# Performance work log

Hardware: AMD Instinct MI355X
Metric: run time of the kernel (lower is better)

The kernel has to match this reference:

```python
import jax, jax.numpy as jnp
import numpy as np

IN_CH = (512, 1024, 512, 256, 256, 256)
CORR = 9          # patch_size of spatial_correlation_sample
UP = 1            # upsample_param
BASE = 96         # level-0 spatial size
B = 2
NEG_SLOPE = 0.01  # nn.LeakyReLU default


def _upsample_nearest(x, s):
    # nearest upsample by integer factor s (matches nn.Upsample(mode='nearest'))
    if s == 1:
        return x
    return jnp.repeat(jnp.repeat(x, s, axis=2), s, axis=3)


def _downsample_nearest(x, s):
    # nearest 'upsample' with scale 1/s: out[d] = in[d*s]
    if s == 1:
        return x
    return x[:, :, ::s, ::s]


def _spatial_correlation(f1, f2, patch):
    # kernel_size=1, stride=1, padding=0, dilation_patch=1, zero pad for
    # out-of-bounds displacements. Returns [b, patch*patch, h, w]
    r = patch // 2
    b, c, h, w = f1.shape
    f2p = jnp.pad(f2, ((0, 0), (0, 0), (r, r), (r, r)))
    vols = [jnp.einsum('bchw,bchw->bhw', f1, f2p[:, :, di:di + h, dj:dj + w])
            for di in range(patch) for dj in range(patch)]
    return jnp.stack(vols, axis=1)


def _forward(xs, xps):
    outs = []
    for i, (feat1, feat2) in enumerate(zip(xs, xps)):
        s = UP * (2 ** i)
        up1 = _upsample_nearest(feat1, s)
        up2 = _upsample_nearest(feat2, s)
        corr = _spatial_correlation(up1, up2, CORR)          # [b, 81, H, W]
        corr = jnp.where(corr >= 0, corr, NEG_SLOPE * corr)  # LeakyReLU
        dw = _downsample_nearest(corr, s)
        dw = dw / jnp.max(dw)                                # global max-normalize
        outs += [dw, corr]
    return tuple(outs)  # flattened list of (dw_corr_feat, corr_feat) pairs


def setup_inputs() -> dict:
    key = jax.random.key(0)
    ks = jax.random.split(key, 12)
    sizes = [BASE // (2 ** i) for i in range(6)]
    inp = {}
    for i in range(6):
        shp = (B, IN_CH[i], sizes[i], sizes[i])
        inp[f'x{i}'] = jax.random.normal(ks[i], shp, dtype=jnp.float32)
        inp[f'xp{i}'] = jax.random.normal(ks[6 + i], shp, dtype=jnp.float32)
    inp['motion_state'] = jnp.zeros((6,), dtype=jnp.float32)  # consumed by zip, never read
    return inp


def reference(x0, x1, x2, x3, x4, x5, xp0, xp1, xp2, xp3, xp4, xp5, motion_state):
    return _forward((x0, x1, x2, x3, x4, x5), (xp0, xp1, xp2, xp3, xp4, xp5))
```

## Files before the change

### kernel.cpp

```cpp
#include <hip/hip_runtime.h>
#include <hip/hip_bf16.h>

#define CEIL(a, b) (((a) + (b) - 1) / (b))

typedef __hip_bfloat16 bf16;
typedef __attribute__((ext_vector_type(2))) _Float16 h16x2;


__global__ __launch_bounds__(64) void k_corr0s(
    const float* __restrict__ f1, const float* __restrict__ f2,
    bf16* __restrict__ part) {
  const int l = threadIdx.x;
  const int flat =
      (int)(blockIdx.x + 2 * (blockIdx.y + 96 * blockIdx.z));
  const int g = flat & 7;
  const int j0 = flat >> 3;
  const int y = g * 12 + (j0 % 12);
  const int rest = j0 / 12;
  const int xt = rest & 1;
  const int zz = rest >> 1;
  const int gc = zz >> 1;
  const int b = zz & 1;
  const int x0 = xt * 48;

  float acc[9][9];
#pragma unroll
  for (int j = 0; j < 9; ++j)
#pragma unroll
    for (int i = 0; i < 9; ++i) acc[j][i] = 0.f;

  const int xa = x0 - 4 + l;
  const bool ok_a = (l < 56) && (xa >= 0) && (xa < 96);
  const int aoff = y * 96 + (xa < 0 ? 0 : (xa > 95 ? 95 : xa));
  const int xv = x0 + (l < 48 ? l : 47);
  bool okv[9];
  int voff[9];
#pragma unroll
  for (int t = 0; t < 9; ++t) {
    int yy = y - 4 + t;
    okv[t] = (l < 48) && (yy >= 0) && (yy < 96);
    voff[t] = (yy < 0 ? 0 : (yy > 95 ? 95 : yy)) * 96 + xv;
  }

  const float* f1b = f1 + (size_t)b * 512 * 9216;
  const float* f2b = f2 + (size_t)b * 512 * 9216;
  const int c0 = gc * 64;
  for (int c = c0; c < c0 + 64; c += 2) {
    float a0 = f1b[(size_t)c * 9216 + aoff];
    float a1 = f1b[(size_t)(c + 1) * 9216 + aoff];
    unsigned au =
        __builtin_bit_cast(unsigned, __builtin_amdgcn_cvt_pkrtz(a0, a1));
    au = ok_a ? au : 0u;
    unsigned asu[9];
#pragma unroll
    for (int i = 0; i < 9; ++i)
      asu[i] = (i == 8) ? au : (unsigned)__shfl((int)au, l + 8 - i);
    unsigned vus[9];
#pragma unroll
    for (int t = 0; t < 9; ++t) {
      float v0 = f2b[(size_t)c * 9216 + voff[t]];
      float v1 = f2b[(size_t)(c + 1) * 9216 + voff[t]];
      unsigned vu =
          __builtin_bit_cast(unsigned, __builtin_amdgcn_cvt_pkrtz(v0, v1));
      vus[t] = okv[t] ? vu : 0u;
    }
#pragma unroll
    for (int j = 0; j < 9; ++j) {
      h16x2 vp = __builtin_bit_cast(h16x2, vus[j]);
#pragma unroll
      for (int i = 0; i < 9; ++i)
        acc[j][i] = __builtin_amdgcn_fdot2(
            __builtin_bit_cast(h16x2, asu[i]), vp, acc[j][i], false);
    }
  }

  if (l < 48) {
    size_t base = ((size_t)((gc * 2 + b) * 96 + y)) * 7776 + x0 + l;
#pragma unroll
    for (int j = 0; j < 9; ++j)
#pragma unroll
      for (int i = 0; i < 9; ++i)
        part[base + (size_t)(j * 9 + i) * 96] = __float2bfloat16(acc[j][i]);
  }
}

__global__ __launch_bounds__(256) void k_corr0red(
    const bf16* __restrict__ part, float* __restrict__ corr0,
    float* __restrict__ maxbuf) {
  const int t = blockIdx.x * 256 + threadIdx.x;
  const int x = t % 96;
  const int y = (t / 96) % 96;
  const int d = (t / 9216) % 81;
  const int b = t / 746496;
  const int dx = d % 9;
  const int xs = x + dx - 4;
  float v = 0.f;
  if (xs >= 0 && xs < 96) {
    size_t base = ((size_t)(b * 96 + y)) * 7776 + (size_t)d * 96 + xs;
    const size_t gstride = (size_t)2 * 96 * 7776;
#pragma unroll
    for (int gc = 0; gc < 8; ++gc)
      v += __bfloat162float(part[base + gc * gstride]);
  }
  v = v >= 0.f ? v : 0.01f * v;
  corr0[t] = v;
  float mx = v;
#pragma unroll
  for (int off = 32; off; off >>= 1) mx = fmaxf(mx, __shfl_down(mx, off));
  __shared__ float wm[4];
  if ((threadIdx.x & 63) == 0) wm[threadIdx.x >> 6] = mx;
  __syncthreads();
  if (threadIdx.x == 0)
    maxbuf[blockIdx.x] = fmaxf(fmaxf(wm[0], wm[1]), fmaxf(wm[2], wm[3]));
}

__global__ __launch_bounds__(64) void k_lc1p(
    const float* __restrict__ f1, const float* __restrict__ f2,
    float* __restrict__ part) {
  const int X = threadIdx.x;
  const int Y = blockIdx.x;
  const int gc = blockIdx.y;
  const int b = blockIdx.z;
  const bool xin = (X < 48);

  float acc2[5][5];
#pragma unroll
  for (int i = 0; i < 5; ++i)
#pragma unroll
    for (int j = 0; j < 5; ++j) acc2[i][j] = 0.f;

  bool okdy[5];
  int voff[5];
#pragma unroll
  for (int dy = 0; dy < 5; ++dy) {
    int YY = Y + dy - 2;
    okdy[dy] = (YY >= 0 && YY < 48) && xin;
    voff[dy] = (YY < 0 ? 0 : (YY > 47 ? 47 : YY)) * 48 + (xin ? X : 0);
  }
  const float* p1 = f1 + (size_t)b * 1024 * 2304 + Y * 48;
  const float* p2 = f2 + (size_t)b * 1024 * 2304;

  const int c0 = gc * 32;
#pragma unroll 2
  for (int c = c0; c < c0 + 32; c += 2) {
    float a0 = xin ? p1[(size_t)c * 2304 + X] : 0.f;
    float a1 = xin ? p1[(size_t)(c + 1) * 2304 + X] : 0.f;
    unsigned au =
        __builtin_bit_cast(unsigned, __builtin_amdgcn_cvt_pkrtz(a0, a1));
    unsigned asu[5];
#pragma unroll
    for (int dx = 0; dx < 5; ++dx) {
      int src = X - dx + 2;
      src = src < 0 ? 0 : (src > 63 ? 63 : src);
      asu[dx] = (dx == 2) ? au : (unsigned)__shfl((int)au, src);
    }
#pragma unroll
    for (int dy = 0; dy < 5; ++dy) {
      float v0 = p2[(size_t)c * 2304 + voff[dy]];
      float v1 = p2[(size_t)(c + 1) * 2304 + voff[dy]];
      unsigned vu =
          __builtin_bit_cast(unsigned, __builtin_amdgcn_cvt_pkrtz(v0, v1));
      vu = okdy[dy] ? vu : 0u;
      h16x2 vp = __builtin_bit_cast(h16x2, vu);
#pragma unroll
      for (int dx = 0; dx < 5; ++dx)
        acc2[dy][dx] = __builtin_amdgcn_fdot2(
            __builtin_bit_cast(h16x2, asu[dx]), vp, acc2[dy][dx], false);
    }
  }

  float* pb = part + ((size_t)(gc * 2 + b) * 25) * 2304 + Y * 48;
#pragma unroll
  for (int dy = 0; dy < 5; ++dy)
#pragma unroll
    for (int dx = 0; dx < 5; ++dx) {
      int src = X + dx - 2;
      int scl = src < 0 ? 0 : (src > 63 ? 63 : src);
      float val = __shfl(acc2[dy][dx], scl);
      bool okx = (X + dx - 2 >= 0) && (X + dx - 2 < 48);
      bool oky = (Y + dy - 2 >= 0) && (Y + dy - 2 < 48);
      if (xin)
        pb[(size_t)(dy * 5 + dx) * 2304 + X] = (oky && okx) ? val : 0.f;
    }
}

__global__ __launch_bounds__(64) void k_lcrow_all(
    const float* __restrict__ x2, const float* __restrict__ q2,
    const float* __restrict__ x3, const float* __restrict__ q3,
    const float* __restrict__ x4, const float* __restrict__ q4,
    const float* __restrict__ x5, const float* __restrict__ q5,
    float* __restrict__ out) {
  int bx = blockIdx.x;
  int S, C, RW;
  const float *f1, *f2;
  float* part;
  if (bx < 12) {
    S = 24; C = 512; RW = 2; f1 = x2; f2 = q2; part = out + 200000;
  } else if (bx < 15) {
    bx -= 12; S = 12; C = 256; RW = 5; f1 = x3; f2 = q3; part = out + 600000;
  } else if (bx < 16) {
    bx -= 15; S = 6; C = 256; RW = 10; f1 = x4; f2 = q4; part = out + 700000;
  } else {
    bx -= 16; S = 3; C = 256; RW = 21; f1 = x5; f2 = q5; part = out + 730000;
  }
  const int cpg = C / 32;
  const int lane = threadIdx.x;
  const int SS = S * S;
  const int yr = lane / S;
  const int X = lane % S;
  const int y = bx * RW + yr;
  const int gc = blockIdx.y;
  const int b = blockIdx.z;
  const bool act = (yr < RW) && (y < S);

  float acc[3][3];
#pragma unroll
  for (int i = 0; i < 3; ++i)
#pragma unroll
    for (int j = 0; j < 3; ++j) acc[i][j] = 0.f;

  bool okdx[3], okdy[3];
  int off1[3], off2[3];
#pragma unroll
  for (int i = 0; i < 3; ++i) {
    int xs = X + 1 - i;
    okdx[i] = act && (xs >= 0) && (xs < S);
    off1[i] = (act ? y : 0) * S + (xs < 0 ? 0 : (xs >= S ? S - 1 : xs));
    int yy = y + i - 1;
    okdy[i] = act && (yy >= 0) && (yy < S);
    off2[i] = (yy < 0 ? 0 : (yy >= S ? S - 1 : yy)) * S + X;
  }

  const float* f1b = f1 + (size_t)b * C * SS;
  const float* f2b = f2 + (size_t)b * C * SS;
  const int c0 = gc * cpg;
  for (int c = c0; c < c0 + cpg; c += 2) {
    const float* p = f1b + (size_t)c * SS;
    const float* pn = p + SS;
    const float* q = f2b + (size_t)c * SS;
    const float* qn = q + SS;
    unsigned au[3], vu[3];
#pragma unroll
    for (int i = 0; i < 3; ++i) {
      unsigned u = __builtin_bit_cast(
          unsigned, __builtin_amdgcn_cvt_pkrtz(p[off1[i]], pn[off1[i]]));
      au[i] = okdx[i] ? u : 0u;
      unsigned w = __builtin_bit_cast(
          unsigned, __builtin_amdgcn_cvt_pkrtz(q[off2[i]], qn[off2[i]]));
      vu[i] = okdy[i] ? w : 0u;
    }
#pragma unroll
    for (int dy = 0; dy < 3; ++dy) {
      h16x2 vp = __builtin_bit_cast(h16x2, vu[dy]);
#pragma unroll
      for (int dxi = 0; dxi < 3; ++dxi)
        acc[dy][dxi] = __builtin_amdgcn_fdot2(
            __builtin_bit_cast(h16x2, au[dxi]), vp, acc[dy][dxi], false);
    }
  }

  if (act) {
    size_t base = ((size_t)(gc * 2 + b) * S + y) * 9 * S + X;
#pragma unroll
    for (int dy = 0; dy < 3; ++dy)
#pragma unroll
      for (int dxi = 0; dxi < 3; ++dxi)
        part[base + (size_t)(dy * 3 + dxi) * S] = acc[dy][dxi];
  }
}

__global__ __launch_bounds__(256) void k_red_all(float* __restrict__ out) {
  int t = blockIdx.x * 256 + threadIdx.x;
  if (t < 115200) {
    const float* part = out + 3359232;
    const int o = t / 4608;
    const int pix = t % 4608;
    const int b = pix / 2304, r = pix % 2304;
    float s = 0.f;
#pragma unroll
    for (int g = 0; g < 32; ++g)
      s += part[((size_t)(g * 2 + b) * 25 + o) * 2304 + r];
    out[(size_t)pix * 25 + o] = s;
    return;
  }
  t -= 115200;
  int S;
  const float* part;
  float* lc;
  if (t < 10368) {
    S = 24; part = out + 200000; lc = out + 115200;
  } else if ((t -= 10368) < 2592) {
    S = 12; part = out + 600000; lc = out + 125568;
  } else if ((t -= 2592) < 648) {
    S = 6; part = out + 700000; lc = out + 128160;
  } else if ((t -= 648) < 162) {
    S = 3; part = out + 730000; lc = out + 128808;
  } else {
    return;
  }
  const int SS = S * S;
  const int o = t % 9;
  const int p = t / 9;
  const int b = p / SS, r = p % SS, y = r / S, X = r % S;
  const int dy = o / 3, dx = o % 3;
  const int xs = X + dx - 1;
  float v = 0.f;
  if (xs >= 0 && xs < S) {
    size_t base = ((size_t)b * S + y) * 9 * S + (size_t)(dy * 3 + dx) * S + xs;
    const size_t gstride = (size_t)2 * S * 9 * S;
#pragma unroll
    for (int g = 0; g < 32; ++g) v += part[base + g * gstride];
  }
  lc[(size_t)p * 9 + o] = v;
}

__global__ __launch_bounds__(256) void k_expand_all(
    float* __restrict__ out, float* __restrict__ maxbuf) {
  static const int lcoffs[6] = {0, 0, 115200, 125568, 128160, 128808};
  static const size_t dwo[6] = {0,       2985984, 4852224,
                                6438528, 7954848, 9453672};
  static const size_t cro[6] = {1492992, 3359232, 4945536,
                                6461856, 7960680, 9455130};
  const int lvl = (int)blockIdx.y + 1;
  const int R = (lvl == 1) ? 2 : 1;
  const float* lc = out + lcoffs[lvl];
  float* out_corr = out + cro[lvl];
  float* out_dw = out + dwo[lvl];
  const int t = blockIdx.x * 256 + threadIdx.x;
  float contrib = 0.f;
  {
    const int x = t % 96;
    const int y = (t / 96) % 96;
    const int d = (t / 9216) % 81;
    const int b = t / 746496;
    const int hy = y + d / 9 - 4;
    const int hx = x + d % 9 - 4;
    float val = 0.f;
    if (hy >= 0 && hy < 96 && hx >= 0 && hx < 96) {
      const int S = 96 >> lvl;
      const int Y1 = y >> lvl, X1 = x >> lvl;
      const int oy = (hy >> lvl) - Y1 + R;
      const int ox = (hx >> lvl) - X1 + R;
      const int DD = 2 * R + 1;
      val = lc[(((size_t)(b * S + Y1) * S + X1) * DD + oy) * DD + ox];
      val = val >= 0.f ? val : 0.01f * val;
    }
    out_corr[t] = val;
    const int m = (1 << lvl) - 1;
    if (((y | x) & m) == 0) {
      const int S = 96 >> lvl;
      out_dw[((size_t)(b * 81 + d) * S + (y >> lvl)) * S + (x >> lvl)] = val;
      contrib = val;
    }
  }
#pragma unroll
  for (int off = 32; off; off >>= 1)
    contrib = fmaxf(contrib, __shfl_down(contrib, off));
  __shared__ float wm[4];
  if ((threadIdx.x & 63) == 0) wm[threadIdx.x >> 6] = contrib;
  __syncthreads();
  if (threadIdx.x == 0)
    maxbuf[(size_t)lvl * 5832 + blockIdx.x] =
        fmaxf(fmaxf(wm[0], wm[1]), fmaxf(wm[2], wm[3]));
}

__global__ __launch_bounds__(1024) void k_finmax(
    const float* __restrict__ maxbuf, unsigned int* __restrict__ slots) {
  const int lvl = blockIdx.x;
  const float* mb = maxbuf + (size_t)lvl * 5832;
  float m = 0.f;
  for (int i = threadIdx.x; i < 5832; i += 1024) m = fmaxf(m, mb[i]);
#pragma unroll
  for (int off = 32; off; off >>= 1) m = fmaxf(m, __shfl_down(m, off));
  __shared__ float wm[16];
  if ((threadIdx.x & 63) == 0) wm[threadIdx.x >> 6] = m;
  __syncthreads();
  if (threadIdx.x == 0) {
    float r = wm[0];
#pragma unroll
    for (int i = 1; i < 16; ++i) r = fmaxf(r, wm[i]);
    slots[lvl] = (unsigned int)__float_as_int(r);
  }
}

__global__ __launch_bounds__(256) void k_norm_all(
    float* __restrict__ out, const unsigned int* __restrict__ slots) {
  int i = blockIdx.x * 256 + threadIdx.x;
  int lvl;
  size_t dst, src;
  if (i < 1492986) {
    lvl = 0; dst = i; src = (size_t)1492992 + i;
  } else if ((i -= 1492986) < 373248) {
    lvl = 1; dst = (size_t)2985984 + i; src = dst;
  } else if ((i -= 373248) < 93312) {
    lvl = 2; dst = (size_t)4852224 + i; src = dst;
  } else if ((i -= 93312) < 23328) {
    lvl = 3; dst = (size_t)6438528 + i; src = dst;
  } else if ((i -= 23328) < 5832) {
    lvl = 4; dst = (size_t)7954848 + i; src = dst;
  } else if ((i -= 5832) < 1458) {
    lvl = 5; dst = (size_t)9453672 + i; src = dst;
  } else {
    return;
  }
  const float m = __int_as_float((int)slots[lvl]);
  out[dst] = out[src] / m;
}

__global__ __launch_bounds__(64) void k_norm0_tail(
    float* __restrict__ out, const unsigned int* __restrict__ slots) {
  const float m = __int_as_float((int)slots[0]);
  if (threadIdx.x < 6) {
    const int t = 1492986 + threadIdx.x;
    out[t] = out[1492992 + t] / m;
  }
}

extern "C" void kernel_launch(void* const* d_in, const int* in_sizes, int n_in,
                              void* d_out, int out_size, void* d_ws,
                              size_t ws_size, hipStream_t stream) {
  const float* x[6];
  const float* xp[6];
  for (int i = 0; i < 6; ++i) {
    x[i] = (const float*)d_in[2 * i];
    xp[i] = (const float*)d_in[2 * i + 1];
  }
  float* out = (float*)d_out;

  float* maxbuf = out + 1400000;
  unsigned int* slots = (unsigned int*)(out + 1492986);
  bf16* part0 = (bf16*)(out + 2985984);
  float* part1 = out + 3359232;

  const int NORM_TOTAL = 1492986 + 373248 + 93312 + 23328 + 5832 + 1458;

  k_corr0s<<<dim3(2, 96, 16), dim3(64), 0, stream>>>(x[0], xp[0], part0);
  k_corr0red<<<dim3(5832), dim3(256), 0, stream>>>(part0, out + 1492992,
                                                   maxbuf);
  k_lc1p<<<dim3(48, 32, 2), dim3(64), 0, stream>>>(x[1], xp[1], part1);
  k_lcrow_all<<<dim3(17, 32, 2), dim3(64), 0, stream>>>(
      x[2], xp[2], x[3], xp[3], x[4], xp[4], x[5], xp[5], out);
  k_red_all<<<dim3(CEIL(128970, 256)), dim3(256), 0, stream>>>(out);
  k_expand_all<<<dim3(5832, 5), dim3(256), 0, stream>>>(out, maxbuf);
  k_finmax<<<dim3(6), dim3(1024), 0, stream>>>(maxbuf, slots);
  k_norm_all<<<dim3(CEIL(NORM_TOTAL, 256)), dim3(256), 0, stream>>>(out,
                                                                    slots);
  k_norm0_tail<<<dim3(1), dim3(64), 0, stream>>>(out, slots);
}
```

Baseline: 116.4 us.

## Merge all partial-correlation kernels and reductions into two launches, store level-1 partials as bf16

The three partial-correlation kernels (level 0, level 1, levels 2-5) become one kernel that dispatches on a flat block index, and the level-0 reduction is merged with the other-level reduction into one kernel. This drops three launches and lets the small-level blocks run alongside the level-0 blocks instead of waiting for them. Level-1 partials are now stored as bf16 in a new scratch region, halving that write/read traffic at some cost in accumulation precision.

```diff
diff --git a/kernel.cpp b/kernel.cpp
--- a/kernel.cpp
+++ b/kernel.cpp
@@ -7,279 +7,280 @@
 typedef __attribute__((ext_vector_type(2))) _Float16 h16x2;
 
 
-__global__ __launch_bounds__(64) void k_corr0s(
-    const float* __restrict__ f1, const float* __restrict__ f2,
-    bf16* __restrict__ part) {
-  const int l = threadIdx.x;
-  const int flat =
-      (int)(blockIdx.x + 2 * (blockIdx.y + 96 * blockIdx.z));
-  const int g = flat & 7;
-  const int j0 = flat >> 3;
-  const int y = g * 12 + (j0 % 12);
-  const int rest = j0 / 12;
-  const int xt = rest & 1;
-  const int zz = rest >> 1;
-  const int gc = zz >> 1;
-  const int b = zz & 1;
-  const int x0 = xt * 48;
-
-  float acc[9][9];
-#pragma unroll
-  for (int j = 0; j < 9; ++j)
-#pragma unroll
-    for (int i = 0; i < 9; ++i) acc[j][i] = 0.f;
-
-  const int xa = x0 - 4 + l;
-  const bool ok_a = (l < 56) && (xa >= 0) && (xa < 96);
-  const int aoff = y * 96 + (xa < 0 ? 0 : (xa > 95 ? 95 : xa));
-  const int xv = x0 + (l < 48 ? l : 47);
-  bool okv[9];
-  int voff[9];
-#pragma unroll
-  for (int t = 0; t < 9; ++t) {
-    int yy = y - 4 + t;
-    okv[t] = (l < 48) && (yy >= 0) && (yy < 96);
-    voff[t] = (yy < 0 ? 0 : (yy > 95 ? 95 : yy)) * 96 + xv;
-  }
-
-  const float* f1b = f1 + (size_t)b * 512 * 9216;
-  const float* f2b = f2 + (size_t)b * 512 * 9216;
-  const int c0 = gc * 64;
-  for (int c = c0; c < c0 + 64; c += 2) {
-    float a0 = f1b[(size_t)c * 9216 + aoff];
-    float a1 = f1b[(size_t)(c + 1) * 9216 + aoff];
-    unsigned au =
-        __builtin_bit_cast(unsigned, __builtin_amdgcn_cvt_pkrtz(a0, a1));
-    au = ok_a ? au : 0u;
-    unsigned asu[9];
-#pragma unroll
-    for (int i = 0; i < 9; ++i)
-      asu[i] = (i == 8) ? au : (unsigned)__shfl((int)au, l + 8 - i);
-    unsigned vus[9];
-#pragma unroll
-    for (int t = 0; t < 9; ++t) {
-      float v0 = f2b[(size_t)c * 9216 + voff[t]];
-      float v1 = f2b[(size_t)(c + 1) * 9216 + voff[t]];
-      unsigned vu =
-          __builtin_bit_cast(unsigned, __builtin_amdgcn_cvt_pkrtz(v0, v1));
-      vus[t] = okv[t] ? vu : 0u;
-    }
-#pragma unroll
-    for (int j = 0; j < 9; ++j) {
-      h16x2 vp = __builtin_bit_cast(h16x2, vus[j]);
-#pragma unroll
-      for (int i = 0; i < 9; ++i)
-        acc[j][i] = __builtin_amdgcn_fdot2(
-            __builtin_bit_cast(h16x2, asu[i]), vp, acc[j][i], false);
-    }
-  }
-
-  if (l < 48) {
-    size_t base = ((size_t)((gc * 2 + b) * 96 + y)) * 7776 + x0 + l;
-#pragma unroll
-    for (int j = 0; j < 9; ++j)
-#pragma unroll
-      for (int i = 0; i < 9; ++i)
-        part[base + (size_t)(j * 9 + i) * 96] = __float2bfloat16(acc[j][i]);
-  }
-}
-
-__global__ __launch_bounds__(256) void k_corr0red(
-    const bf16* __restrict__ part, float* __restrict__ corr0,
-    float* __restrict__ maxbuf) {
-  const int t = blockIdx.x * 256 + threadIdx.x;
-  const int x = t % 96;
-  const int y = (t / 96) % 96;
-  const int d = (t / 9216) % 81;
-  const int b = t / 746496;
-  const int dx = d % 9;
-  const int xs = x + dx - 4;
-  float v = 0.f;
-  if (xs >= 0 && xs < 96) {
-    size_t base = ((size_t)(b * 96 + y)) * 7776 + (size_t)d * 96 + xs;
-    const size_t gstride = (size_t)2 * 96 * 7776;
-#pragma unroll
-    for (int gc = 0; gc < 8; ++gc)
-      v += __bfloat162float(part[base + gc * gstride]);
-  }
-  v = v >= 0.f ? v : 0.01f * v;
-  corr0[t] = v;
-  float mx = v;
-#pragma unroll
-  for (int off = 32; off; off >>= 1) mx = fmaxf(mx, __shfl_down(mx, off));
-  __shared__ float wm[4];
-  if ((threadIdx.x & 63) == 0) wm[threadIdx.x >> 6] = mx;
-  __syncthreads();
-  if (threadIdx.x == 0)
-    maxbuf[blockIdx.x] = fmaxf(fmaxf(wm[0], wm[1]), fmaxf(wm[2], wm[3]));
-}
-
-__global__ __launch_bounds__(64) void k_lc1p(
-    const float* __restrict__ f1, const float* __restrict__ f2,
-    float* __restrict__ part) {
-  const int X = threadIdx.x;
-  const int Y = blockIdx.x;
-  const int gc = blockIdx.y;
-  const int b = blockIdx.z;
-  const bool xin = (X < 48);
-
-  float acc2[5][5];
-#pragma unroll
-  for (int i = 0; i < 5; ++i)
-#pragma unroll
-    for (int j = 0; j < 5; ++j) acc2[i][j] = 0.f;
-
-  bool okdy[5];
-  int voff[5];
-#pragma unroll
-  for (int dy = 0; dy < 5; ++dy) {
-    int YY = Y + dy - 2;
-    okdy[dy] = (YY >= 0 && YY < 48) && xin;
-    voff[dy] = (YY < 0 ? 0 : (YY > 47 ? 47 : YY)) * 48 + (xin ? X : 0);
-  }
-  const float* p1 = f1 + (size_t)b * 1024 * 2304 + Y * 48;
-  const float* p2 = f2 + (size_t)b * 1024 * 2304;
-
-  const int c0 = gc * 32;
-#pragma unroll 2
-  for (int c = c0; c < c0 + 32; c += 2) {
-    float a0 = xin ? p1[(size_t)c * 2304 + X] : 0.f;
-    float a1 = xin ? p1[(size_t)(c + 1) * 2304 + X] : 0.f;
-    unsigned au =
-        __builtin_bit_cast(unsigned, __builtin_amdgcn_cvt_pkrtz(a0, a1));
-    unsigned asu[5];
-#pragma unroll
-    for (int dx = 0; dx < 5; ++dx) {
-      int src = X - dx + 2;
-      src = src < 0 ? 0 : (src > 63 ? 63 : src);
-      asu[dx] = (dx == 2) ? au : (unsigned)__shfl((int)au, src);
-    }
-#pragma unroll
-    for (int dy = 0; dy < 5; ++dy) {
-      float v0 = p2[(size_t)c * 2304 + voff[dy]];
-      float v1 = p2[(size_t)(c + 1) * 2304 + voff[dy]];
-      unsigned vu =
-          __builtin_bit_cast(unsigned, __builtin_amdgcn_cvt_pkrtz(v0, v1));
-      vu = okdy[dy] ? vu : 0u;
-      h16x2 vp = __builtin_bit_cast(h16x2, vu);
-#pragma unroll
-      for (int dx = 0; dx < 5; ++dx)
-        acc2[dy][dx] = __builtin_amdgcn_fdot2(
-            __builtin_bit_cast(h16x2, asu[dx]), vp, acc2[dy][dx], false);
-    }
-  }
-
-  float* pb = part + ((size_t)(gc * 2 + b) * 25) * 2304 + Y * 48;
-#pragma unroll
-  for (int dy = 0; dy < 5; ++dy)
-#pragma unroll
-    for (int dx = 0; dx < 5; ++dx) {
-      int src = X + dx - 2;
-      int scl = src < 0 ? 0 : (src > 63 ? 63 : src);
-      float val = __shfl(acc2[dy][dx], scl);
-      bool okx = (X + dx - 2 >= 0) && (X + dx - 2 < 48);
-      bool oky = (Y + dy - 2 >= 0) && (Y + dy - 2 < 48);
-      if (xin)
-        pb[(size_t)(dy * 5 + dx) * 2304 + X] = (oky && okx) ? val : 0.f;
-    }
-}
-
-__global__ __launch_bounds__(64) void k_lcrow_all(
+__global__ __launch_bounds__(64) void k_part_all(
+    const float* __restrict__ x0, const float* __restrict__ q0,
+    const float* __restrict__ x1, const float* __restrict__ q1,
     const float* __restrict__ x2, const float* __restrict__ q2,
     const float* __restrict__ x3, const float* __restrict__ q3,
     const float* __restrict__ x4, const float* __restrict__ q4,
     const float* __restrict__ x5, const float* __restrict__ q5,
+    bf16* __restrict__ part0, bf16* __restrict__ part1,
     float* __restrict__ out) {
-  int bx = blockIdx.x;
-  int S, C, RW;
-  const float *f1, *f2;
-  float* part;
-  if (bx < 12) {
-    S = 24; C = 512; RW = 2; f1 = x2; f2 = q2; part = out + 200000;
-  } else if (bx < 15) {
-    bx -= 12; S = 12; C = 256; RW = 5; f1 = x3; f2 = q3; part = out + 600000;
-  } else if (bx < 16) {
-    bx -= 15; S = 6; C = 256; RW = 10; f1 = x4; f2 = q4; part = out + 700000;
+  const int id = blockIdx.x;
+  const int l = threadIdx.x;
+
+  if (id < 3072) {
+    const int flat = id;
+    const int g = flat & 7;
+    const int j0 = flat >> 3;
+    const int y = g * 12 + (j0 % 12);
+    const int rest = j0 / 12;
+    const int xt = rest & 1;
+    const int zz = rest >> 1;
+    const int gc = zz >> 1;
+    const int b = zz & 1;
+    const int x0b = xt * 48;
+
+    float acc[9][9];
+#pragma unroll
+    for (int j = 0; j < 9; ++j)
+#pragma unroll
+      for (int i = 0; i < 9; ++i) acc[j][i] = 0.f;
+
+    const int xa = x0b - 4 + l;
+    const bool ok_a = (l < 56) && (xa >= 0) && (xa < 96);
+    const int aoff = y * 96 + (xa < 0 ? 0 : (xa > 95 ? 95 : xa));
+    const int xv = x0b + (l < 48 ? l : 47);
+    bool okv[9];
+    int voff[9];
+#pragma unroll
+    for (int t = 0; t < 9; ++t) {
+      int yy = y - 4 + t;
+      okv[t] = (l < 48) && (yy >= 0) && (yy < 96);
+      voff[t] = (yy < 0 ? 0 : (yy > 95 ? 95 : yy)) * 96 + xv;
+    }
+
+    const float* f1b = x0 + (size_t)b * 512 * 9216;
+    const float* f2b = q0 + (size_t)b * 512 * 9216;
+    const int c0 = gc * 64;
+    for (int c = c0; c < c0 + 64; c += 2) {
+      float a0 = f1b[(size_t)c * 9216 + aoff];
+      float a1 = f1b[(size_t)(c + 1) * 9216 + aoff];
+      unsigned au =
+          __builtin_bit_cast(unsigned, __builtin_amdgcn_cvt_pkrtz(a0, a1));
+      au = ok_a ? au : 0u;
+      unsigned asu[9];
+#pragma unroll
+      for (int i = 0; i < 9; ++i)
+        asu[i] = (i == 8) ? au : (unsigned)__shfl((int)au, l + 8 - i);
+      unsigned vus[9];
+#pragma unroll
+      for (int t = 0; t < 9; ++t) {
+        float v0 = f2b[(size_t)c * 9216 + voff[t]];
+        float v1 = f2b[(size_t)(c + 1) * 9216 + voff[t]];
+        unsigned vu =
+            __builtin_bit_cast(unsigned, __builtin_amdgcn_cvt_pkrtz(v0, v1));
+        vus[t] = okv[t] ? vu : 0u;
+      }
+#pragma unroll
+      for (int j = 0; j < 9; ++j) {
+        h16x2 vp = __builtin_bit_cast(h16x2, vus[j]);
+#pragma unroll
+        for (int i = 0; i < 9; ++i)
+          acc[j][i] = __builtin_amdgcn_fdot2(
+              __builtin_bit_cast(h16x2, asu[i]), vp, acc[j][i], false);
+      }
+    }
+
+    if (l < 48) {
+      size_t base = ((size_t)((gc * 2 + b) * 96 + y)) * 7776 + x0b + l;
+#pragma unroll
+      for (int j = 0; j < 9; ++j)
+#pragma unroll
+        for (int i = 0; i < 9; ++i)
+          part0[base + (size_t)(j * 9 + i) * 96] = __float2bfloat16(acc[j][i]);
+    }
+  } else if (id < 6144) {
+    const int id2 = id - 3072;
+    const int Y = id2 % 48;
+    const int gg = id2 / 48;
+    const int gc = gg & 31;
+    const int b = gg >> 5;
+    const int X = l;
+    const bool xin = (X < 48);
+
+    float acc2[5][5];
+#pragma unroll
+    for (int i = 0; i < 5; ++i)
+#pragma unroll
+      for (int j = 0; j < 5; ++j) acc2[i][j] = 0.f;
+
+    bool okdy[5];
+    int voff[5];
+#pragma unroll
+    for (int dy = 0; dy < 5; ++dy) {
+      int YY = Y + dy - 2;
+      okdy[dy] = (YY >= 0 && YY < 48) && xin;
+      voff[dy] = (YY < 0 ? 0 : (YY > 47 ? 47 : YY)) * 48 + (xin ? X : 0);
+    }
+    const float* p1 = x1 + (size_t)b * 1024 * 2304 + Y * 48;
+    const float* p2 = q1 + (size_t)b * 1024 * 2304;
+
+    const int c0 = gc * 32;
+#pragma unroll 2
+    for (int c = c0; c < c0 + 32; c += 2) {
+      float a0 = xin ? p1[(size_t)c * 2304 + X] : 0.f;
+      float a1 = xin ? p1[(size_t)(c + 1) * 2304 + X] : 0.f;
+      unsigned au =
+          __builtin_bit_cast(unsigned, __builtin_amdgcn_cvt_pkrtz(a0, a1));
+      unsigned asu[5];
+#pragma unroll
+      for (int dx = 0; dx < 5; ++dx) {
+        int src = X - dx + 2;
+        src = src < 0 ? 0 : (src > 63 ? 63 : src);
+        asu[dx] = (dx == 2) ? au : (unsigned)__shfl((int)au, src);
+      }
+#pragma unroll
+      for (int dy = 0; dy < 5; ++dy) {
+        float v0 = p2[(size_t)c * 2304 + voff[dy]];
+        float v1 = p2[(size_t)(c + 1) * 2304 + voff[dy]];
+        unsigned vu =
+            __builtin_bit_cast(unsigned, __builtin_amdgcn_cvt_pkrtz(v0, v1));
+        vu = okdy[dy] ? vu : 0u;
+        h16x2 vp = __builtin_bit_cast(h16x2, vu);
+#pragma unroll
+        for (int dx = 0; dx < 5; ++dx)
+          acc2[dy][dx] = __builtin_amdgcn_fdot2(
+              __builtin_bit_cast(h16x2, asu[dx]), vp, acc2[dy][dx], false);
+      }
+    }
+
+    bf16* pb = part1 + ((size_t)(gc * 2 + b) * 25) * 2304 + Y * 48;
+#pragma unroll
+    for (int dy = 0; dy < 5; ++dy)
+#pragma unroll
+      for (int dx = 0; dx < 5; ++dx) {
+        int src = X + dx - 2;
+        int scl = src < 0 ? 0 : (src > 63 ? 63 : src);
+        float val = __shfl(acc2[dy][dx], scl);
+        bool okx = (X + dx - 2 >= 0) && (X + dx - 2 < 48);
+        bool oky = (Y + dy - 2 >= 0) && (Y + dy - 2 < 48);
+        if (xin)
+          pb[(size_t)(dy * 5 + dx) * 2304 + X] =
+              __float2bfloat16((oky && okx) ? val : 0.f);
+      }
   } else {
-    bx -= 16; S = 3; C = 256; RW = 21; f1 = x5; f2 = q5; part = out + 730000;
-  }
-  const int cpg = C / 32;
-  const int lane = threadIdx.x;
-  const int SS = S * S;
-  const int yr = lane / S;
-  const int X = lane % S;
-  const int y = bx * RW + yr;
-  const int gc = blockIdx.y;
-  const int b = blockIdx.z;
-  const bool act = (yr < RW) && (y < S);
-
-  float acc[3][3];
-#pragma unroll
-  for (int i = 0; i < 3; ++i)
-#pragma unroll
-    for (int j = 0; j < 3; ++j) acc[i][j] = 0.f;
-
-  bool okdx[3], okdy[3];
-  int off1[3], off2[3];
-#pragma unroll
-  for (int i = 0; i < 3; ++i) {
-    int xs = X + 1 - i;
-    okdx[i] = act && (xs >= 0) && (xs < S);
-    off1[i] = (act ? y : 0) * S + (xs < 0 ? 0 : (xs >= S ? S - 1 : xs));
-    int yy = y + i - 1;
-    okdy[i] = act && (yy >= 0) && (yy < S);
-    off2[i] = (yy < 0 ? 0 : (yy >= S ? S - 1 : yy)) * S + X;
-  }
-
-  const float* f1b = f1 + (size_t)b * C * SS;
-  const float* f2b = f2 + (size_t)b * C * SS;
-  const int c0 = gc * cpg;
-  for (int c = c0; c < c0 + cpg; c += 2) {
-    const float* p = f1b + (size_t)c * SS;
-    const float* pn = p + SS;
-    const float* q = f2b + (size_t)c * SS;
-    const float* qn = q + SS;
-    unsigned au[3], vu[3];
+    const int id3 = id - 6144;
+    int bx = id3 % 17;
+    const int gg = id3 / 17;
+    const int gc = gg & 31;
+    const int b = gg >> 5;
+    int S, C, RW;
+    const float *f1, *f2;
+    float* part;
+    if (bx < 12) {
+      S = 24; C = 512; RW = 2; f1 = x2; f2 = q2; part = out + 200000;
+    } else if (bx < 15) {
+      bx -= 12; S = 12; C = 256; RW = 5; f1 = x3; f2 = q3; part = out + 600000;
+    } else if (bx < 16) {
+      bx -= 15; S = 6; C = 256; RW = 10; f1 = x4; f2 = q4; part = out + 700000;
+    } else {
+      bx -= 16; S = 3; C = 256; RW = 21; f1 = x5; f2 = q5; part = out + 730000;
+    }
+    const int cpg = C / 32;
+    const int SS = S * S;
+    const int yr = l / S;
+    const int X = l % S;
+    const int y = bx * RW + yr;
+    const bool act = (yr < RW) && (y < S);
+
+    float acc[3][3];
+#pragma unroll
+    for (int i = 0; i < 3; ++i)
+#pragma unroll
+      for (int j = 0; j < 3; ++j) acc[i][j] = 0.f;
+
+    bool okdx[3], okdy[3];
+    int off1[3], off2[3];
 #pragma unroll
     for (int i = 0; i < 3; ++i) {
-      unsigned u = __builtin_bit_cast(
-          unsigned, __builtin_amdgcn_cvt_pkrtz(p[off1[i]], pn[off1[i]]));
-      au[i] = okdx[i] ? u : 0u;
-      unsigned w = __builtin_bit_cast(
-          unsigned, __builtin_amdgcn_cvt_pkrtz(q[off2[i]], qn[off2[i]]));
-      vu[i] = okdy[i] ? w : 0u;
-    }
-#pragma unroll
-    for (int dy = 0; dy < 3; ++dy) {
-      h16x2 vp = __builtin_bit_cast(h16x2, vu[dy]);
-#pragma unroll
-      for (int dxi = 0; dxi < 3; ++dxi)
-        acc[dy][dxi] = __builtin_amdgcn_fdot2(
-            __builtin_bit_cast(h16x2, au[dxi]), vp, acc[dy][dxi], false);
-    }
-  }
-
-  if (act) {
-    size_t base = ((size_t)(gc * 2 + b) * S + y) * 9 * S + X;
-#pragma unroll
-    for (int dy = 0; dy < 3; ++dy)
-#pragma unroll
-      for (int dxi = 0; dxi < 3; ++dxi)
-        part[base + (size_t)(dy * 3 + dxi) * S] = acc[dy][dxi];
-  }
-}
-
-__global__ __launch_bounds__(256) void k_red_all(float* __restrict__ out) {
-  int t = blockIdx.x * 256 + threadIdx.x;
+      int xs = X + 1 - i;
+      okdx[i] = act && (xs >= 0) && (xs < S);
+      off1[i] = (act ? y : 0) * S + (xs < 0 ? 0 : (xs >= S ? S - 1 : xs));
+      int yy = y + i - 1;
+      okdy[i] = act && (yy >= 0) && (yy < S);
+      off2[i] = (yy < 0 ? 0 : (yy >= S ? S - 1 : yy)) * S + X;
+    }
+
+    const float* f1b = f1 + (size_t)b * C * SS;
+    const float* f2b = f2 + (size_t)b * C * SS;
+    const int c0 = gc * cpg;
+    for (int c = c0; c < c0 + cpg; c += 2) {
+      const float* p = f1b + (size_t)c * SS;
+      const float* pn = p + SS;
+      const float* q = f2b + (size_t)c * SS;
+      const float* qn = q + SS;
+      unsigned au[3], vu[3];
+#pragma unroll
+      for (int i = 0; i < 3; ++i) {
+        unsigned u = __builtin_bit_cast(
+            unsigned, __builtin_amdgcn_cvt_pkrtz(p[off1[i]], pn[off1[i]]));
+        au[i] = okdx[i] ? u : 0u;
+        unsigned w = __builtin_bit_cast(
+            unsigned, __builtin_amdgcn_cvt_pkrtz(q[off2[i]], qn[off2[i]]));
+        vu[i] = okdy[i] ? w : 0u;
+      }
+#pragma unroll
+      for (int dy = 0; dy < 3; ++dy) {
+        h16x2 vp = __builtin_bit_cast(h16x2, vu[dy]);
+#pragma unroll
+        for (int dxi = 0; dxi < 3; ++dxi)
+          acc[dy][dxi] = __builtin_amdgcn_fdot2(
+              __builtin_bit_cast(h16x2, au[dxi]), vp, acc[dy][dxi], false);
+      }
+    }
+
+    if (act) {
+      size_t base = ((size_t)(gc * 2 + b) * S + y) * 9 * S + X;
+#pragma unroll
+      for (int dy = 0; dy < 3; ++dy)
+#pragma unroll
+        for (int dxi = 0; dxi < 3; ++dxi)
+          part[base + (size_t)(dy * 3 + dxi) * S] = acc[dy][dxi];
+    }
+  }
+}
+
+__global__ __launch_bounds__(256) void k_red2(
+    const bf16* __restrict__ part0, const bf16* __restrict__ part1,
+    float* __restrict__ out, float* __restrict__ maxbuf) {
+  if (blockIdx.x < 5832) {
+    const int t = blockIdx.x * 256 + threadIdx.x;
+    const int x = t % 96;
+    const int y = (t / 96) % 96;
+    const int d = (t / 9216) % 81;
+    const int b = t / 746496;
+    const int dx = d % 9;
+    const int xs = x + dx - 4;
+    float v = 0.f;
+    if (xs >= 0 && xs < 96) {
+      size_t base = ((size_t)(b * 96 + y)) * 7776 + (size_t)d * 96 + xs;
+      const size_t gstride = (size_t)2 * 96 * 7776;
+#pragma unroll
+      for (int gc = 0; gc < 8; ++gc)
+        v += __bfloat162float(part0[base + gc * gstride]);
+    }
+    v = v >= 0.f ? v : 0.01f * v;
+    out[1492992 + t] = v;
+    float mx = v;
+#pragma unroll
+    for (int off = 32; off; off >>= 1) mx = fmaxf(mx, __shfl_down(mx, off));
+    __shared__ float wm[4];
+    if ((threadIdx.x & 63) == 0) wm[threadIdx.x >> 6] = mx;
+    __syncthreads();
+    if (threadIdx.x == 0)
+      maxbuf[blockIdx.x] = fmaxf(fmaxf(wm[0], wm[1]), fmaxf(wm[2], wm[3]));
+    return;
+  }
+  int t = (blockIdx.x - 5832) * 256 + threadIdx.x;
   if (t < 115200) {
-    const float* part = out + 3359232;
     const int o = t / 4608;
     const int pix = t % 4608;
     const int b = pix / 2304, r = pix % 2304;
     float s = 0.f;
 #pragma unroll
     for (int g = 0; g < 32; ++g)
-      s += part[((size_t)(g * 2 + b) * 25 + o) * 2304 + r];
+      s += __bfloat162float(part1[((size_t)(g * 2 + b) * 25 + o) * 2304 + r]);
     out[(size_t)pix * 25 + o] = s;
     return;
   }
@@ -430,17 +431,14 @@
   float* maxbuf = out + 1400000;
   unsigned int* slots = (unsigned int*)(out + 1492986);
   bf16* part0 = (bf16*)(out + 2985984);
-  float* part1 = out + 3359232;
+  bf16* part1 = (bf16*)(out + 8957952);
 
   const int NORM_TOTAL = 1492986 + 373248 + 93312 + 23328 + 5832 + 1458;
 
-  k_corr0s<<<dim3(2, 96, 16), dim3(64), 0, stream>>>(x[0], xp[0], part0);
-  k_corr0red<<<dim3(5832), dim3(256), 0, stream>>>(part0, out + 1492992,
-                                                   maxbuf);
-  k_lc1p<<<dim3(48, 32, 2), dim3(64), 0, stream>>>(x[1], xp[1], part1);
-  k_lcrow_all<<<dim3(17, 32, 2), dim3(64), 0, stream>>>(
-      x[2], xp[2], x[3], xp[3], x[4], xp[4], x[5], xp[5], out);
-  k_red_all<<<dim3(CEIL(128970, 256)), dim3(256), 0, stream>>>(out);
+  k_part_all<<<dim3(7232), dim3(64), 0, stream>>>(
+      x[0], xp[0], x[1], xp[1], x[2], xp[2], x[3], xp[3], x[4], xp[4], x[5],
+      xp[5], part0, part1, out);
+  k_red2<<<dim3(6336), dim3(256), 0, stream>>>(part0, part1, out, maxbuf);
   k_expand_all<<<dim3(5832, 5), dim3(256), 0, stream>>>(out, maxbuf);
   k_finmax<<<dim3(6), dim3(1024), 0, stream>>>(maxbuf, slots);
   k_norm_all<<<dim3(CEIL(NORM_TOTAL, 256)), dim3(256), 0, stream>>>(out,
```

Measured after the change: 106.7 us. 8.3% less time.
